# Kernel optimization log

Measured on AMD Instinct MI355X. Metric: run time of the kernel, lower is better.

Reference implementation:

```python
import jax, jax.numpy as jnp
import numpy as np

N_LAYER = 2
N_HEAD = 16
TOP_K = 2
CAPACITY = 1024  # B*T*top_k/num_experts * capacity_factor = 2*2048*2/8


def layer_norm(x, g, b, eps=1e-5):
    m = jnp.mean(x, axis=-1, keepdims=True)
    v = jnp.var(x, axis=-1, keepdims=True)
    return (x - m) * jax.lax.rsqrt(v + eps) * g + b


def attention(x, qkv_w, out_w):
    B, T, C = x.shape
    H, D = N_HEAD, C // N_HEAD
    qkv = (x @ qkv_w).reshape(B, T, 3, H, D)
    q, k, v = qkv[:, :, 0], qkv[:, :, 1], qkv[:, :, 2]
    scores = jnp.einsum('bthd,bshd->bhts', q, k) / jnp.sqrt(jnp.asarray(D, x.dtype))
    probs = jax.nn.softmax(scores, axis=-1)  # non-causal, dropout=0 (eval)
    o = jnp.einsum('bhts,bshd->bthd', probs, v).reshape(B, T, C)
    return o @ out_w


def sparse_moe(x, route_w, route_b, noise_w, noise_b, w1, b1, w2, b2, key):
    B, T, C = x.shape
    E = route_w.shape[-1]
    N = B * T
    flat = x.reshape(N, C)
    logits = flat @ route_w + route_b
    noise_logits = flat @ noise_w + noise_b
    noise = jax.random.normal(key, logits.shape, logits.dtype) * jax.nn.softplus(noise_logits)
    noisy = logits + noise
    topv, topi = jax.lax.top_k(noisy, TOP_K)            # [N,k]
    probs_k = jax.nn.softmax(topv, axis=-1)             # softmax over sparse(-inf) logits == softmax over top-k
    router = jnp.zeros_like(noisy).at[jnp.arange(N)[:, None], topi].set(probs_k)  # [N,E]
    # dispatch: per-expert token selection in token order, truncated at CAPACITY
    masks = (topi[None] == jnp.arange(E)[:, None, None]).any(-1)  # [E,N]
    order = jnp.argsort(~masks, axis=1, stable=True)[:, :CAPACITY]  # [E,cap] routed tokens first, in order
    valid = jnp.take_along_axis(masks, order, axis=1)               # [E,cap]
    gating = router[order, jnp.arange(E)[:, None]]                  # [E,cap]
    g = flat[order]                                                 # [E,cap,C]
    h = jax.nn.relu(jnp.einsum('ecd,edh->ech', g, w1) + b1[:, None])
    y = jnp.einsum('ech,ehd->ecd', h, w2) + b2[:, None]
    y = y * (gating * valid.astype(x.dtype))[..., None]
    upd = jnp.zeros_like(flat).at[order.reshape(-1)].add(y.reshape(-1, C))
    return upd.reshape(B, T, C)


def setup_inputs() -> dict:
    key = jax.random.key(0)
    ks = jax.random.split(key, 16)
    B, T, C, E, L, V = 2, 2048, 1024, 8, N_LAYER, 32000
    s = lambda fan: 1.0 / np.sqrt(fan)
    return {
        'input_ids': jax.random.randint(ks[0], (B, T), 0, V),
        'tok_emb': jax.random.normal(ks[1], (V, C), jnp.float32) * 0.02,
        'pos_emb': jax.random.normal(ks[2], (T, C), jnp.float32) * 0.02,
        'ln1_g': jnp.ones((L, C), jnp.float32), 'ln1_b': jnp.zeros((L, C), jnp.float32),
        'ln2_g': jnp.ones((L, C), jnp.float32), 'ln2_b': jnp.zeros((L, C), jnp.float32),
        'qkv_w': jax.random.normal(ks[3], (L, C, 3 * C), jnp.float32) * s(C),
        'out_w': jax.random.normal(ks[4], (L, C, C), jnp.float32) * s(C),
        'route_w': jax.random.normal(ks[5], (L, C, E), jnp.float32) * s(C),
        'route_b': jnp.zeros((L, E), jnp.float32),
        'noise_w': jax.random.normal(ks[6], (L, C, E), jnp.float32) * s(C),
        'noise_b': jnp.zeros((L, E), jnp.float32),
        'w1': jax.random.normal(ks[7], (L, E, C, 4 * C), jnp.float32) * s(C),
        'b1': jnp.zeros((L, E, 4 * C), jnp.float32),
        'w2': jax.random.normal(ks[8], (L, E, 4 * C, C), jnp.float32) * s(4 * C),
        'b2': jnp.zeros((L, E, C), jnp.float32),
        'lnf_g': jnp.ones((C,), jnp.float32), 'lnf_b': jnp.zeros((C,), jnp.float32),
        'head_w': jax.random.normal(ks[9], (C, 1), jnp.float32) * s(C),
        'head_b': jnp.zeros((1,), jnp.float32),
    }


def reference(input_ids, tok_emb, pos_emb, ln1_g, ln1_b, ln2_g, ln2_b, qkv_w, out_w,
              route_w, route_b, noise_w, noise_b, w1, b1, w2, b2, lnf_g, lnf_b, head_w, head_b):
    B, T = input_ids.shape
    x = tok_emb[input_ids] + pos_emb[:T]
    base = jax.random.key(42)
    for l in range(N_LAYER):
        x = x + attention(layer_norm(x, ln1_g[l], ln1_b[l]), qkv_w[l], out_w[l])
        moe = sparse_moe(layer_norm(x, ln2_g[l], ln2_b[l]), route_w[l], route_b[l],
                         noise_w[l], noise_b[l], w1[l], b1[l], w2[l], b2[l],
                         jax.random.fold_in(base, l))
        x = x + moe
    x = layer_norm(x, lnf_g, lnf_b)
    return x @ head_w + head_b  # [B,T,1]
```

## Files before the change

kernel.cpp:

```cpp
#include <hip/hip_runtime.h>
#include <stdint.h>
#include <math.h>

#define NTOK 4096
#define TSEQ 2048
#define CDIM 1024
#define NHEAD 16
#define DHEAD 64
#define NEXP 8
#define HIDN 4096
#define ECAP 1024

__device__ __forceinline__ void threefry2x32(uint32_t k0, uint32_t k1,
                                             uint32_t x0, uint32_t x1,
                                             uint32_t& o0, uint32_t& o1) {
  uint32_t ks2 = k0 ^ k1 ^ 0x1BD11BDAu;
#define TF_R(r) { x0 += x1; x1 = (x1 << (r)) | (x1 >> (32 - (r))); x1 ^= x0; }
  x0 += k0; x1 += k1;
  TF_R(13) TF_R(15) TF_R(26) TF_R(6)
  x0 += k1; x1 += ks2 + 1u;
  TF_R(17) TF_R(29) TF_R(16) TF_R(24)
  x0 += ks2; x1 += k0 + 2u;
  TF_R(13) TF_R(15) TF_R(26) TF_R(6)
  x0 += k0; x1 += k1 + 3u;
  TF_R(17) TF_R(29) TF_R(16) TF_R(24)
  x0 += k1; x1 += ks2 + 4u;
  TF_R(13) TF_R(15) TF_R(26) TF_R(6)
  x0 += ks2; x1 += k0 + 5u;
#undef TF_R
  o0 = x0; o1 = x1;
}

__device__ __forceinline__ float erfinv_f32(float x) {
  float w = -log1pf(-x * x);
  float p;
  if (w < 5.0f) {
    w = w - 2.5f;
    p = 2.81022636e-08f;
    p = fmaf(p, w, 3.43273939e-07f);
    p = fmaf(p, w, -3.5233877e-06f);
    p = fmaf(p, w, -4.39150654e-06f);
    p = fmaf(p, w, 0.00021858087f);
    p = fmaf(p, w, -0.00125372503f);
    p = fmaf(p, w, -0.00417768164f);
    p = fmaf(p, w, 0.246640727f);
    p = fmaf(p, w, 1.50140941f);
  } else {
    w = sqrtf(w) - 3.0f;
    p = -0.000200214257f;
    p = fmaf(p, w, 0.000100950558f);
    p = fmaf(p, w, 0.00134934322f);
    p = fmaf(p, w, -0.00367342844f);
    p = fmaf(p, w, 0.00573950773f);
    p = fmaf(p, w, -0.0076224613f);
    p = fmaf(p, w, 0.00943887047f);
    p = fmaf(p, w, 1.00167406f);
    p = fmaf(p, w, 2.83297682f);
  }
  return p * x;
}

__global__ __launch_bounds__(256) void k_embed(const int* __restrict__ ids,
    const float* __restrict__ tok, const float* __restrict__ pos,
    float* __restrict__ x) {
  int row = blockIdx.x;
  int id = ids[row];
  int t = row & (TSEQ - 1);
  const float* tr = tok + (size_t)id * CDIM;
  const float* pr = pos + (size_t)t * CDIM;
  float* xr = x + (size_t)row * CDIM;
  for (int c = threadIdx.x; c < CDIM; c += 256) xr[c] = tr[c] + pr[c];
}

__global__ __launch_bounds__(256) void k_ln(const float* __restrict__ in,
    float* __restrict__ out, const float* __restrict__ g, const float* __restrict__ b) {
  __shared__ float red[256];
  int row = blockIdx.x, tid = threadIdx.x;
  const float* xr = in + (size_t)row * CDIM;
  float s = 0.f;
  for (int c = tid; c < CDIM; c += 256) s += xr[c];
  red[tid] = s; __syncthreads();
  for (int off = 128; off > 0; off >>= 1) {
    if (tid < off) red[tid] += red[tid + off];
    __syncthreads();
  }
  float m = red[0] * (1.0f / CDIM);
  __syncthreads();
  float v = 0.f;
  for (int c = tid; c < CDIM; c += 256) { float d = xr[c] - m; v += d * d; }
  red[tid] = v; __syncthreads();
  for (int off = 128; off > 0; off >>= 1) {
    if (tid < off) red[tid] += red[tid + off];
    __syncthreads();
  }
  float var = red[0] * (1.0f / CDIM);
  float rstd = 1.0f / sqrtf(var + 1e-5f);
  float* orow = out + (size_t)row * CDIM;
  for (int c = tid; c < CDIM; c += 256)
    orow[c] = (xr[c] - m) * rstd * g[c] + b[c];
}

__global__ __launch_bounds__(256, 2) void k_gemm(
    const float* __restrict__ A, int lda,
    const float* __restrict__ B, int ldb,
    float* __restrict__ Cm, int ldc,
    int M, int N, int K,
    const float* __restrict__ bias,
    const int* __restrict__ gather,
    const int* __restrict__ countPtr,
    int flags,
    size_t zsA, size_t zsB, size_t zsC, int zsBias, int zsGather) {
  __shared__ float As[16][132];
  __shared__ float Bs[16][128];
  const int z = blockIdx.z;
  A += (size_t)z * zsA;
  B += (size_t)z * zsB;
  Cm += (size_t)z * zsC;
  if (bias) bias += (size_t)z * (size_t)zsBias;
  if (gather) gather += (size_t)z * (size_t)zsGather;
  int Meff = M;
  if (countPtr) { int cc = countPtr[z]; if (cc < Meff) Meff = cc; }
  const int row0 = blockIdx.y << 7, col0 = blockIdx.x << 7;
  if (row0 >= Meff) return;
  const int tid = threadIdx.x;
  const int tx = tid & 15, ty = tid >> 4;
  const int r0 = ty << 2, c0 = tx << 2;

  const int am0 = tid >> 2, ak0 = (tid & 3) << 2;
  const int am1 = am0 + 64, ak1 = ak0;
  const int bk0 = tid >> 5, bn0 = (tid & 31) << 2;
  const int bk1 = bk0 + 8,  bn1 = bn0;

  const int ag0 = row0 + am0, ag1 = row0 + am1;
  const float* aP0 = nullptr; const float* aP1 = nullptr;
  if (ag0 < Meff) aP0 = A + (size_t)(gather ? gather[ag0] : ag0) * lda + ak0;
  if (ag1 < Meff) aP1 = A + (size_t)(gather ? gather[ag1] : ag1) * lda + ak1;
  const float* bP0 = B + (size_t)bk0 * ldb + col0 + bn0;
  const float* bP1 = B + (size_t)bk1 * ldb + col0 + bn1;

  const float4 z4 = make_float4(0.f, 0.f, 0.f, 0.f);
  float4 aR0 = aP0 ? *(const float4*)aP0 : z4;
  float4 aR1 = aP1 ? *(const float4*)aP1 : z4;
  float4 bR0 = *(const float4*)bP0;
  float4 bR1 = *(const float4*)bP1;

  float acc[8][8];
#pragma unroll
  for (int i = 0; i < 8; ++i)
#pragma unroll
    for (int j = 0; j < 8; ++j) acc[i][j] = 0.f;

  for (int k0 = 0; k0 < K; k0 += 16) {
    As[ak0 + 0][am0] = aR0.x; As[ak0 + 1][am0] = aR0.y;
    As[ak0 + 2][am0] = aR0.z; As[ak0 + 3][am0] = aR0.w;
    As[ak1 + 0][am1] = aR1.x; As[ak1 + 1][am1] = aR1.y;
    As[ak1 + 2][am1] = aR1.z; As[ak1 + 3][am1] = aR1.w;
    *(float4*)&Bs[bk0][bn0] = bR0;
    *(float4*)&Bs[bk1][bn1] = bR1;
    __syncthreads();
    const int kn = k0 + 16;
    if (kn < K) {
      aR0 = aP0 ? *(const float4*)(aP0 + kn) : z4;
      aR1 = aP1 ? *(const float4*)(aP1 + kn) : z4;
      bR0 = *(const float4*)(bP0 + (size_t)kn * ldb);
      bR1 = *(const float4*)(bP1 + (size_t)kn * ldb);
    }
#pragma unroll
    for (int kk = 0; kk < 16; ++kk) {
      const float4 A0 = *(const float4*)&As[kk][r0];
      const float4 A1 = *(const float4*)&As[kk][r0 + 64];
      const float4 B0 = *(const float4*)&Bs[kk][c0];
      const float4 B1 = *(const float4*)&Bs[kk][c0 + 64];
      const float a[8] = {A0.x, A0.y, A0.z, A0.w, A1.x, A1.y, A1.z, A1.w};
      const float b[8] = {B0.x, B0.y, B0.z, B0.w, B1.x, B1.y, B1.z, B1.w};
#pragma unroll
      for (int i = 0; i < 8; ++i)
#pragma unroll
        for (int j = 0; j < 8; ++j) acc[i][j] = fmaf(a[i], b[j], acc[i][j]);
    }
    __syncthreads();
  }

#pragma unroll
  for (int ih = 0; ih < 2; ++ih) {
#pragma unroll
    for (int i = 0; i < 4; ++i) {
      int gr = row0 + r0 + ih * 64 + i;
      if (gr >= Meff) continue;
      float* crow = Cm + (size_t)gr * ldc + col0;
#pragma unroll
      for (int jh = 0; jh < 2; ++jh) {
        int cc = c0 + jh * 64;
        float4 v;
        v.x = acc[ih * 4 + i][jh * 4 + 0];
        v.y = acc[ih * 4 + i][jh * 4 + 1];
        v.z = acc[ih * 4 + i][jh * 4 + 2];
        v.w = acc[ih * 4 + i][jh * 4 + 3];
        if (bias) {
          v.x += bias[col0 + cc + 0]; v.y += bias[col0 + cc + 1];
          v.z += bias[col0 + cc + 2]; v.w += bias[col0 + cc + 3];
        }
        if (flags & 1) {
          v.x = fmaxf(v.x, 0.f); v.y = fmaxf(v.y, 0.f);
          v.z = fmaxf(v.z, 0.f); v.w = fmaxf(v.w, 0.f);
        }
        if (flags & 2) {
          float4 o = *(const float4*)&crow[cc];
          v.x += o.x; v.y += o.y; v.z += o.z; v.w += o.w;
        }
        *(float4*)&crow[cc] = v;
      }
    }
  }
}

__global__ __launch_bounds__(256, 1) void k_attn(const float* __restrict__ qkv,
                                                 float* __restrict__ o) {
  __shared__ float Qs[64][132];
  __shared__ float Ks[64][66];
  __shared__ float Vs[64][68];
  __shared__ float Ps[64][132];
  const int t0 = blockIdx.x << 7;
  const int h = blockIdx.y;
  const int b = blockIdx.z;
  const int tid = threadIdx.x;
  const int tx = tid & 15, ty = tid >> 4;
  const int r0 = ty << 2;
  const int c0 = tx << 2;

#pragma unroll
  for (int p = 0; p < 8; ++p) {
    int idx = tid + (p << 8);
    int r = idx >> 4, d4 = (idx & 15) << 2;
    const float4 q = *(const float4*)(qkv +
        ((size_t)(b * TSEQ + t0 + r) * 3 + 0) * CDIM + h * DHEAD + d4);
    Qs[d4 + 0][r] = q.x * 0.125f;
    Qs[d4 + 1][r] = q.y * 0.125f;
    Qs[d4 + 2][r] = q.z * 0.125f;
    Qs[d4 + 3][r] = q.w * 0.125f;
  }

  float m0[8], l0[8], Oacc[8][4];
#pragma unroll
  for (int i = 0; i < 8; ++i) {
    m0[i] = -INFINITY; l0[i] = 0.f;
#pragma unroll
    for (int j = 0; j < 4; ++j) Oacc[i][j] = 0.f;
  }

  float4 kreg[4], vreg[4];
#pragma unroll
  for (int p = 0; p < 4; ++p) {
    int idx = tid + (p << 8);
    int j = idx >> 4, d4 = (idx & 15) << 2;
    kreg[p] = *(const float4*)(qkv + ((size_t)(b * TSEQ + j) * 3 + 1) * CDIM + h * DHEAD + d4);
    vreg[p] = *(const float4*)(qkv + ((size_t)(b * TSEQ + j) * 3 + 2) * CDIM + h * DHEAD + d4);
  }

  for (int s0 = 0; s0 < TSEQ; s0 += 64) {
#pragma unroll
    for (int p = 0; p < 4; ++p) {
      int idx = tid + (p << 8);
      int j = idx >> 4, d4 = (idx & 15) << 2;
      Ks[d4 + 0][j] = kreg[p].x;
      Ks[d4 + 1][j] = kreg[p].y;
      Ks[d4 + 2][j] = kreg[p].z;
      Ks[d4 + 3][j] = kreg[p].w;
      *(float4*)&Vs[j][d4] = vreg[p];
    }
    __syncthreads();
    if (s0 + 64 < TSEQ) {
#pragma unroll
      for (int p = 0; p < 4; ++p) {
        int idx = tid + (p << 8);
        int j = idx >> 4, d4 = (idx & 15) << 2;
        kreg[p] = *(const float4*)(qkv + ((size_t)(b * TSEQ + s0 + 64 + j) * 3 + 1) * CDIM + h * DHEAD + d4);
        vreg[p] = *(const float4*)(qkv + ((size_t)(b * TSEQ + s0 + 64 + j) * 3 + 2) * CDIM + h * DHEAD + d4);
      }
    }
    float sacc[8][4];
#pragma unroll
    for (int i = 0; i < 8; ++i)
#pragma unroll
      for (int j = 0; j < 4; ++j) sacc[i][j] = 0.f;
#pragma unroll 8
    for (int kk = 0; kk < 64; ++kk) {
      const float4 qa = *(const float4*)&Qs[kk][r0];
      const float4 qb = *(const float4*)&Qs[kk][r0 + 64];
      const float2 ka = *(const float2*)&Ks[kk][c0];
      const float2 kb = *(const float2*)&Ks[kk][c0 + 2];
      const float av[8] = {qa.x, qa.y, qa.z, qa.w, qb.x, qb.y, qb.z, qb.w};
      const float bv[4] = {ka.x, ka.y, kb.x, kb.y};
#pragma unroll
      for (int i = 0; i < 8; ++i)
#pragma unroll
        for (int j = 0; j < 4; ++j) sacc[i][j] = fmaf(av[i], bv[j], sacc[i][j]);
    }
    float pv[8][4];
#pragma unroll
    for (int i = 0; i < 8; ++i) {
      float mx = fmaxf(fmaxf(sacc[i][0], sacc[i][1]), fmaxf(sacc[i][2], sacc[i][3]));
#pragma unroll
      for (int off = 8; off > 0; off >>= 1) mx = fmaxf(mx, __shfl_xor(mx, off, 16));
      float mnew = fmaxf(m0[i], mx);
      float alpha = expf(m0[i] - mnew);
      float psum = 0.f;
#pragma unroll
      for (int j = 0; j < 4; ++j) {
        float p = expf(sacc[i][j] - mnew);
        pv[i][j] = p;
        psum += p;
      }
#pragma unroll
      for (int off = 8; off > 0; off >>= 1) psum += __shfl_xor(psum, off, 16);
      l0[i] = l0[i] * alpha + psum;
      m0[i] = mnew;
#pragma unroll
      for (int j = 0; j < 4; ++j) Oacc[i][j] *= alpha;
    }
#pragma unroll
    for (int jj = 0; jj < 4; ++jj) {
      *(float4*)&Ps[c0 + jj][r0] =
          make_float4(pv[0][jj], pv[1][jj], pv[2][jj], pv[3][jj]);
      *(float4*)&Ps[c0 + jj][r0 + 64] =
          make_float4(pv[4][jj], pv[5][jj], pv[6][jj], pv[7][jj]);
    }
    __syncthreads();
#pragma unroll 8
    for (int kk = 0; kk < 64; ++kk) {
      const float4 pa = *(const float4*)&Ps[kk][r0];
      const float4 pb = *(const float4*)&Ps[kk][r0 + 64];
      const float4 vv = *(const float4*)&Vs[kk][c0];
      const float av[8] = {pa.x, pa.y, pa.z, pa.w, pb.x, pb.y, pb.z, pb.w};
      const float bv[4] = {vv.x, vv.y, vv.z, vv.w};
#pragma unroll
      for (int i = 0; i < 8; ++i)
#pragma unroll
        for (int j = 0; j < 4; ++j) Oacc[i][j] = fmaf(av[i], bv[j], Oacc[i][j]);
    }
    __syncthreads();
  }
#pragma unroll
  for (int i = 0; i < 8; ++i) {
    int r = t0 + ((i < 4) ? (r0 + i) : (r0 + 60 + i));
    float inv = 1.0f / l0[i];
    float4 v;
    v.x = Oacc[i][0] * inv; v.y = Oacc[i][1] * inv;
    v.z = Oacc[i][2] * inv; v.w = Oacc[i][3] * inv;
    *(float4*)(o + (size_t)(b * TSEQ + r) * CDIM + h * DHEAD + c0) = v;
  }
}

__global__ __launch_bounds__(256) void k_route(
    const float* __restrict__ xn,
    const float* __restrict__ rw, const float* __restrict__ rb,
    const float* __restrict__ nw, const float* __restrict__ nb,
    int layer, int* __restrict__ topi, float* __restrict__ gate) {
  int token = blockIdx.x, tid = threadIdx.x;
  float acc[16];
#pragma unroll
  for (int j = 0; j < 16; j++) acc[j] = 0.f;
  const float* xr = xn + (size_t)token * CDIM;
  for (int c = tid; c < CDIM; c += 256) {
    float xc = xr[c];
    const float* w1p = rw + (size_t)c * NEXP;
    const float* w2p = nw + (size_t)c * NEXP;
#pragma unroll
    for (int j = 0; j < 8; j++) acc[j] += xc * w1p[j];
#pragma unroll
    for (int j = 0; j < 8; j++) acc[8 + j] += xc * w2p[j];
  }
#pragma unroll
  for (int j = 0; j < 16; j++) {
#pragma unroll
    for (int off = 32; off > 0; off >>= 1) acc[j] += __shfl_xor(acc[j], off, 64);
  }
  __shared__ float wp[4][16];
  int wid = tid >> 6;
  if ((tid & 63) == 0) {
#pragma unroll
    for (int j = 0; j < 16; j++) wp[wid][j] = acc[j];
  }
  __syncthreads();
  __shared__ float noisy[8];
  if (tid < 8) {
    int j = tid;
    float logit = wp[0][j] + wp[1][j] + wp[2][j] + wp[3][j] + rb[j];
    float nl = wp[0][8 + j] + wp[1][8 + j] + wp[2][8 + j] + wp[3][8 + j] + nb[j];
    float sp = fmaxf(nl, 0.f) + log1pf(expf(-fabsf(nl)));
    uint32_t k0, k1, o0, o1;
    threefry2x32(0u, 42u, 0u, (uint32_t)layer, k0, k1);
    uint32_t idx = (uint32_t)(token * NEXP + j);
    threefry2x32(k0, k1, 0u, idx, o0, o1);
    uint32_t bits = o0 ^ o1;
    float f = __uint_as_float((bits >> 9) | 0x3f800000u) - 1.0f;
    const float lo = -0.99999994f;
    float u = fmaxf(lo, f * 2.0f + lo);
    float z = 1.41421356f * erfinv_f32(u);
    noisy[j] = logit + z * sp;
  }
  __syncthreads();
  if (tid == 0) {
    float v1 = -INFINITY; int i1 = 0;
#pragma unroll
    for (int j = 0; j < 8; j++) { float v = noisy[j]; if (v > v1) { v1 = v; i1 = j; } }
    float v2 = -INFINITY; int i2 = 0;
#pragma unroll
    for (int j = 0; j < 8; j++) {
      if (j == i1) continue;
      float v = noisy[j]; if (v > v2) { v2 = v; i2 = j; }
    }
    float e2 = expf(v2 - v1);
    float denom = 1.0f + e2;
    topi[token * 2] = i1; topi[token * 2 + 1] = i2;
    gate[token * 2] = 1.0f / denom;
    gate[token * 2 + 1] = e2 / denom;
  }
}

__global__ __launch_bounds__(256) void k_scan(const int* __restrict__ topi,
    int* __restrict__ perm, int* __restrict__ slot, int* __restrict__ count) {
  int e = blockIdx.x, tid = threadIdx.x;
  __shared__ int ps[256];
  __shared__ int sbase;
  if (tid == 0) sbase = 0;
  __syncthreads();
  for (int c0 = 0; c0 < NTOK; c0 += 256) {
    int token = c0 + tid;
    int j0 = topi[token * 2], j1 = topi[token * 2 + 1];
    int flag = (j0 == e || j1 == e) ? 1 : 0;
    ps[tid] = flag;
    __syncthreads();
    for (int off = 1; off < 256; off <<= 1) {
      int v = (tid >= off) ? ps[tid - off] : 0;
      __syncthreads();
      ps[tid] += v;
      __syncthreads();
    }
    int pos = sbase + ps[tid] - flag;
    if (flag) {
      int s = (pos < ECAP) ? pos : -1;
      if (s >= 0) perm[e * ECAP + s] = token;
      if (j0 == e) slot[token * 2] = s;
      else slot[token * 2 + 1] = s;
    }
    __syncthreads();
    if (tid == 0) sbase += ps[255];
    __syncthreads();
  }
  if (tid == 0) count[e] = (sbase < ECAP) ? sbase : ECAP;
}

__global__ __launch_bounds__(256) void k_moe_add(
    const float* __restrict__ ybuf,
    const int* __restrict__ topi, const int* __restrict__ slot,
    const float* __restrict__ gate, float* __restrict__ x) {
  int token = blockIdx.x, tid = threadIdx.x;
  int e0 = topi[token * 2], s0 = slot[token * 2];
  int e1 = topi[token * 2 + 1], s1 = slot[token * 2 + 1];
  float g0 = gate[token * 2], g1 = gate[token * 2 + 1];
  const float* y0 = ybuf + ((size_t)e0 * ECAP + (s0 < 0 ? 0 : s0)) * CDIM;
  const float* y1 = ybuf + ((size_t)e1 * ECAP + (s1 < 0 ? 0 : s1)) * CDIM;
  float* xr = x + (size_t)token * CDIM;
  for (int c = tid; c < CDIM; c += 256) {
    float v = xr[c];
    if (s0 >= 0) v += g0 * y0[c];
    if (s1 >= 0) v += g1 * y1[c];
    xr[c] = v;
  }
}

__global__ __launch_bounds__(256) void k_head(const float* __restrict__ xn,
    const float* __restrict__ hw, const float* __restrict__ hb,
    float* __restrict__ out) {
  __shared__ float red[256];
  int token = blockIdx.x, tid = threadIdx.x;
  const float* xr = xn + (size_t)token * CDIM;
  float s = 0.f;
  for (int c = tid; c < CDIM; c += 256) s += xr[c] * hw[c];
  red[tid] = s; __syncthreads();
  for (int off = 128; off > 0; off >>= 1) {
    if (tid < off) red[tid] += red[tid + off];
    __syncthreads();
  }
  if (tid == 0) out[token] = red[0] + hb[0];
}

extern "C" void kernel_launch(void* const* d_in, const int* in_sizes, int n_in,
                              void* d_out, int out_size, void* d_ws, size_t ws_size,
                              hipStream_t stream) {
  const int* ids = (const int*)d_in[0];
  const float* tok_emb = (const float*)d_in[1];
  const float* pos_emb = (const float*)d_in[2];
  const float* ln1_g = (const float*)d_in[3];
  const float* ln1_b = (const float*)d_in[4];
  const float* ln2_g = (const float*)d_in[5];
  const float* ln2_b = (const float*)d_in[6];
  const float* qkv_w = (const float*)d_in[7];
  const float* out_w = (const float*)d_in[8];
  const float* route_w = (const float*)d_in[9];
  const float* route_b = (const float*)d_in[10];
  const float* noise_w = (const float*)d_in[11];
  const float* noise_b = (const float*)d_in[12];
  const float* w1 = (const float*)d_in[13];
  const float* b1 = (const float*)d_in[14];
  const float* w2 = (const float*)d_in[15];
  const float* b2 = (const float*)d_in[16];
  const float* lnf_g = (const float*)d_in[17];
  const float* lnf_b = (const float*)d_in[18];
  const float* head_w = (const float*)d_in[19];
  const float* head_b = (const float*)d_in[20];
  float* out = (float*)d_out;

  const size_t MB = 1024u * 1024u;
  char* ws = (char*)d_ws;
  const bool big = ws_size >= (size_t)194 * MB;

  float* x    = (float*)(ws);
  float* xn   = (float*)(ws + 16 * MB);
  float* qkv  = (float*)(ws + 32 * MB);
  float* hbuf = (float*)(ws + 32 * MB);
  float* ybuf = big ? (float*)(ws + 160 * MB)
                    : (float*)(ws + 48 * MB);
  char* small = big ? (ws + 192 * MB) : (ws + 80 * MB);
  int* topi = (int*)small;
  int* slot = topi + 2 * NTOK;
  float* gate = (float*)(slot + 2 * NTOK);
  int* perm = (int*)(gate + 2 * NTOK);
  int* count = perm + NEXP * ECAP;

  k_embed<<<NTOK, 256, 0, stream>>>(ids, tok_emb, pos_emb, x);

  for (int l = 0; l < 2; l++) {
    k_ln<<<NTOK, 256, 0, stream>>>(x, xn, ln1_g + l * CDIM, ln1_b + l * CDIM);
    k_gemm<<<dim3(3 * CDIM / 128, NTOK / 128, 1), 256, 0, stream>>>(xn, CDIM,
        qkv_w + (size_t)l * CDIM * 3 * CDIM, 3 * CDIM, qkv, 3 * CDIM,
        NTOK, 3 * CDIM, CDIM, nullptr, nullptr, nullptr, 0,
        0, 0, 0, 0, 0);
    k_attn<<<dim3(TSEQ / 128, NHEAD, 2), 256, 0, stream>>>(qkv, xn);
    k_gemm<<<dim3(CDIM / 128, NTOK / 128, 1), 256, 0, stream>>>(xn, CDIM,
        out_w + (size_t)l * CDIM * CDIM, CDIM, x, CDIM,
        NTOK, CDIM, CDIM, nullptr, nullptr, nullptr, 2,
        0, 0, 0, 0, 0);
    k_ln<<<NTOK, 256, 0, stream>>>(x, xn, ln2_g + l * CDIM, ln2_b + l * CDIM);
    k_route<<<NTOK, 256, 0, stream>>>(xn,
        route_w + (size_t)l * CDIM * NEXP, route_b + l * NEXP,
        noise_w + (size_t)l * CDIM * NEXP, noise_b + l * NEXP,
        l, topi, gate);
    k_scan<<<NEXP, 256, 0, stream>>>(topi, perm, slot, count);
    if (big) {
      k_gemm<<<dim3(HIDN / 128, ECAP / 128, NEXP), 256, 0, stream>>>(xn, CDIM,
          w1 + (size_t)l * NEXP * CDIM * HIDN, HIDN, hbuf, HIDN,
          ECAP, HIDN, CDIM, b1 + (size_t)l * NEXP * HIDN, perm, count, 1,
          0, (size_t)CDIM * HIDN, (size_t)ECAP * HIDN, HIDN, ECAP);
      k_gemm<<<dim3(CDIM / 128, ECAP / 128, NEXP), 256, 0, stream>>>(hbuf, HIDN,
          w2 + (size_t)l * NEXP * HIDN * CDIM, CDIM, ybuf, CDIM,
          ECAP, CDIM, HIDN, b2 + (size_t)l * NEXP * CDIM, nullptr, count, 0,
          (size_t)ECAP * HIDN, (size_t)HIDN * CDIM, (size_t)ECAP * CDIM, CDIM, 0);
    } else {
      for (int e = 0; e < NEXP; e++) {
        const size_t we = (size_t)(l * NEXP + e);
        k_gemm<<<dim3(HIDN / 128, ECAP / 128, 1), 256, 0, stream>>>(xn, CDIM,
            w1 + we * CDIM * HIDN, HIDN, hbuf, HIDN,
            ECAP, HIDN, CDIM, b1 + we * HIDN, perm + e * ECAP, count + e, 1,
            0, 0, 0, 0, 0);
        k_gemm<<<dim3(CDIM / 128, ECAP / 128, 1), 256, 0, stream>>>(hbuf, HIDN,
            w2 + we * HIDN * CDIM, CDIM, ybuf + (size_t)e * ECAP * CDIM, CDIM,
            ECAP, CDIM, HIDN, b2 + we * CDIM, nullptr, count + e, 0,
            0, 0, 0, 0, 0);
      }
    }
    k_moe_add<<<NTOK, 256, 0, stream>>>(ybuf, topi, slot, gate, x);
  }

  k_ln<<<NTOK, 256, 0, stream>>>(x, xn, lnf_g, lnf_b);
  k_head<<<NTOK, 256, 0, stream>>>(xn, head_w, head_b, out);
}
```

Before: 5.856 ms.

## Use split-bf16 MFMA (3-pass) in GEMM kernel instead of FP32 FMA

Replaces the FP32 SIMT outer-product GEMM with matrix-core MFMA 16x16x32 bf16 instructions. Each FP32 operand is split into a bf16 high and low part, and three products (hh, hl, lh) are accumulated to approximate FP32 precision. Shared-memory tiles are reorganised into k-contiguous bf16 layouts with a K step of 32. The aim is to move the dominant GEMM cost onto the matrix cores. In exchange, accuracy drops slightly relative to exact FP32, and the epilogue now writes scalars instead of float4 stores.

```diff
diff --git a/kernel.cpp b/kernel.cpp
--- a/kernel.cpp
+++ b/kernel.cpp
@@ -10,6 +10,9 @@
 #define NEXP 8
 #define HIDN 4096
 #define ECAP 1024
+
+typedef short bf16x8 __attribute__((ext_vector_type(8)));
+typedef float f32x4 __attribute__((ext_vector_type(4)));
 
 __device__ __forceinline__ void threefry2x32(uint32_t k0, uint32_t k1,
                                              uint32_t x0, uint32_t x1,
@@ -60,6 +63,16 @@
   return p * x;
 }
 
+__device__ __forceinline__ void split2(float x0, float x1,
+                                       uint32_t& hi, uint32_t& lo) {
+  uint32_t h, l;
+  asm("v_cvt_pk_bf16_f32 %0, %1, %2" : "=v"(h) : "v"(x0), "v"(x1));
+  float h0 = __uint_as_float(h << 16);
+  float h1 = __uint_as_float(h & 0xffff0000u);
+  asm("v_cvt_pk_bf16_f32 %0, %1, %2" : "=v"(l) : "v"(x0 - h0), "v"(x1 - h1));
+  hi = h; lo = l;
+}
+
 __global__ __launch_bounds__(256) void k_embed(const int* __restrict__ ids,
     const float* __restrict__ tok, const float* __restrict__ pos,
     float* __restrict__ x) {
@@ -110,8 +123,10 @@
     const int* __restrict__ countPtr,
     int flags,
     size_t zsA, size_t zsB, size_t zsC, int zsBias, int zsGather) {
-  __shared__ float As[16][132];
-  __shared__ float Bs[16][128];
+  __shared__ short Ah[128][40];
+  __shared__ short Al[128][40];
+  __shared__ short Bh[128][40];
+  __shared__ short Bl[128][40];
   const int z = blockIdx.z;
   A += (size_t)z * zsA;
   B += (size_t)z * zsB;
@@ -123,92 +138,111 @@
   const int row0 = blockIdx.y << 7, col0 = blockIdx.x << 7;
   if (row0 >= Meff) return;
   const int tid = threadIdx.x;
-  const int tx = tid & 15, ty = tid >> 4;
-  const int r0 = ty << 2, c0 = tx << 2;
-
-  const int am0 = tid >> 2, ak0 = (tid & 3) << 2;
-  const int am1 = am0 + 64, ak1 = ak0;
-  const int bk0 = tid >> 5, bn0 = (tid & 31) << 2;
-  const int bk1 = bk0 + 8,  bn1 = bn0;
-
-  const int ag0 = row0 + am0, ag1 = row0 + am1;
-  const float* aP0 = nullptr; const float* aP1 = nullptr;
-  if (ag0 < Meff) aP0 = A + (size_t)(gather ? gather[ag0] : ag0) * lda + ak0;
-  if (ag1 < Meff) aP1 = A + (size_t)(gather ? gather[ag1] : ag1) * lda + ak1;
-  const float* bP0 = B + (size_t)bk0 * ldb + col0 + bn0;
-  const float* bP1 = B + (size_t)bk1 * ldb + col0 + bn1;
+
+  const int ar = tid >> 1, ak = (tid & 1) << 4;
+  const int bk = (tid >> 5) << 2, bc = (tid & 31) << 2;
+
+  const int agrow = row0 + ar;
+  const float* aP = nullptr;
+  if (agrow < Meff) aP = A + (size_t)(gather ? gather[agrow] : agrow) * lda + ak;
+  const float* bP = B + (size_t)bk * ldb + col0 + bc;
 
   const float4 z4 = make_float4(0.f, 0.f, 0.f, 0.f);
-  float4 aR0 = aP0 ? *(const float4*)aP0 : z4;
-  float4 aR1 = aP1 ? *(const float4*)aP1 : z4;
-  float4 bR0 = *(const float4*)bP0;
-  float4 bR1 = *(const float4*)bP1;
-
-  float acc[8][8];
-#pragma unroll
-  for (int i = 0; i < 8; ++i)
-#pragma unroll
-    for (int j = 0; j < 8; ++j) acc[i][j] = 0.f;
-
-  for (int k0 = 0; k0 < K; k0 += 16) {
-    As[ak0 + 0][am0] = aR0.x; As[ak0 + 1][am0] = aR0.y;
-    As[ak0 + 2][am0] = aR0.z; As[ak0 + 3][am0] = aR0.w;
-    As[ak1 + 0][am1] = aR1.x; As[ak1 + 1][am1] = aR1.y;
-    As[ak1 + 2][am1] = aR1.z; As[ak1 + 3][am1] = aR1.w;
-    *(float4*)&Bs[bk0][bn0] = bR0;
-    *(float4*)&Bs[bk1][bn1] = bR1;
-    __syncthreads();
-    const int kn = k0 + 16;
+  float4 aR[4], bR[4];
+#pragma unroll
+  for (int j = 0; j < 4; ++j) {
+    aR[j] = aP ? *(const float4*)(aP + (j << 2)) : z4;
+    bR[j] = *(const float4*)(bP + (size_t)j * ldb);
+  }
+
+  const int lane = tid & 63, wv = tid >> 6;
+  const int wr = (wv >> 1) << 6, wc = (wv & 1) << 6;
+  const int lr = lane & 15;
+  const int k8 = (lane >> 4) << 3;
+  const int qrow = (lane >> 4) << 2;
+
+  f32x4 acc[4][4];
+#pragma unroll
+  for (int i = 0; i < 4; ++i)
+#pragma unroll
+    for (int j = 0; j < 4; ++j) acc[i][j] = (f32x4)0.f;
+
+  for (int k0 = 0; k0 < K; k0 += 32) {
+    {
+      uint32_t h[8], l[8];
+      split2(aR[0].x, aR[0].y, h[0], l[0]);
+      split2(aR[0].z, aR[0].w, h[1], l[1]);
+      split2(aR[1].x, aR[1].y, h[2], l[2]);
+      split2(aR[1].z, aR[1].w, h[3], l[3]);
+      split2(aR[2].x, aR[2].y, h[4], l[4]);
+      split2(aR[2].z, aR[2].w, h[5], l[5]);
+      split2(aR[3].x, aR[3].y, h[6], l[6]);
+      split2(aR[3].z, aR[3].w, h[7], l[7]);
+      *(uint4*)&Ah[ar][ak]     = make_uint4(h[0], h[1], h[2], h[3]);
+      *(uint4*)&Ah[ar][ak + 8] = make_uint4(h[4], h[5], h[6], h[7]);
+      *(uint4*)&Al[ar][ak]     = make_uint4(l[0], l[1], l[2], l[3]);
+      *(uint4*)&Al[ar][ak + 8] = make_uint4(l[4], l[5], l[6], l[7]);
+    }
+    {
+      uint32_t h01, l01, h23, l23;
+      split2(bR[0].x, bR[1].x, h01, l01); split2(bR[2].x, bR[3].x, h23, l23);
+      *(uint2*)&Bh[bc + 0][bk] = make_uint2(h01, h23);
+      *(uint2*)&Bl[bc + 0][bk] = make_uint2(l01, l23);
+      split2(bR[0].y, bR[1].y, h01, l01); split2(bR[2].y, bR[3].y, h23, l23);
+      *(uint2*)&Bh[bc + 1][bk] = make_uint2(h01, h23);
+      *(uint2*)&Bl[bc + 1][bk] = make_uint2(l01, l23);
+      split2(bR[0].z, bR[1].z, h01, l01); split2(bR[2].z, bR[3].z, h23, l23);
+      *(uint2*)&Bh[bc + 2][bk] = make_uint2(h01, h23);
+      *(uint2*)&Bl[bc + 2][bk] = make_uint2(l01, l23);
+      split2(bR[0].w, bR[1].w, h01, l01); split2(bR[2].w, bR[3].w, h23, l23);
+      *(uint2*)&Bh[bc + 3][bk] = make_uint2(h01, h23);
+      *(uint2*)&Bl[bc + 3][bk] = make_uint2(l01, l23);
+    }
+    __syncthreads();
+    const int kn = k0 + 32;
     if (kn < K) {
-      aR0 = aP0 ? *(const float4*)(aP0 + kn) : z4;
-      aR1 = aP1 ? *(const float4*)(aP1 + kn) : z4;
-      bR0 = *(const float4*)(bP0 + (size_t)kn * ldb);
-      bR1 = *(const float4*)(bP1 + (size_t)kn * ldb);
-    }
-#pragma unroll
-    for (int kk = 0; kk < 16; ++kk) {
-      const float4 A0 = *(const float4*)&As[kk][r0];
-      const float4 A1 = *(const float4*)&As[kk][r0 + 64];
-      const float4 B0 = *(const float4*)&Bs[kk][c0];
-      const float4 B1 = *(const float4*)&Bs[kk][c0 + 64];
-      const float a[8] = {A0.x, A0.y, A0.z, A0.w, A1.x, A1.y, A1.z, A1.w};
-      const float b[8] = {B0.x, B0.y, B0.z, B0.w, B1.x, B1.y, B1.z, B1.w};
-#pragma unroll
-      for (int i = 0; i < 8; ++i)
-#pragma unroll
-        for (int j = 0; j < 8; ++j) acc[i][j] = fmaf(a[i], b[j], acc[i][j]);
-    }
-    __syncthreads();
-  }
-
-#pragma unroll
-  for (int ih = 0; ih < 2; ++ih) {
-#pragma unroll
-    for (int i = 0; i < 4; ++i) {
-      int gr = row0 + r0 + ih * 64 + i;
-      if (gr >= Meff) continue;
-      float* crow = Cm + (size_t)gr * ldc + col0;
-#pragma unroll
-      for (int jh = 0; jh < 2; ++jh) {
-        int cc = c0 + jh * 64;
-        float4 v;
-        v.x = acc[ih * 4 + i][jh * 4 + 0];
-        v.y = acc[ih * 4 + i][jh * 4 + 1];
-        v.z = acc[ih * 4 + i][jh * 4 + 2];
-        v.w = acc[ih * 4 + i][jh * 4 + 3];
-        if (bias) {
-          v.x += bias[col0 + cc + 0]; v.y += bias[col0 + cc + 1];
-          v.z += bias[col0 + cc + 2]; v.w += bias[col0 + cc + 3];
-        }
-        if (flags & 1) {
-          v.x = fmaxf(v.x, 0.f); v.y = fmaxf(v.y, 0.f);
-          v.z = fmaxf(v.z, 0.f); v.w = fmaxf(v.w, 0.f);
-        }
-        if (flags & 2) {
-          float4 o = *(const float4*)&crow[cc];
-          v.x += o.x; v.y += o.y; v.z += o.z; v.w += o.w;
-        }
-        *(float4*)&crow[cc] = v;
+#pragma unroll
+      for (int j = 0; j < 4; ++j) {
+        aR[j] = aP ? *(const float4*)(aP + kn + (j << 2)) : z4;
+        bR[j] = *(const float4*)(bP + (size_t)(kn + j) * ldb);
+      }
+    }
+    bf16x8 vbh[4], vbl[4];
+#pragma unroll
+    for (int nt = 0; nt < 4; ++nt) {
+      vbh[nt] = *(const bf16x8*)&Bh[wc + nt * 16 + lr][k8];
+      vbl[nt] = *(const bf16x8*)&Bl[wc + nt * 16 + lr][k8];
+    }
+#pragma unroll
+    for (int mt = 0; mt < 4; ++mt) {
+      const bf16x8 vah = *(const bf16x8*)&Ah[wr + mt * 16 + lr][k8];
+      const bf16x8 val = *(const bf16x8*)&Al[wr + mt * 16 + lr][k8];
+#pragma unroll
+      for (int nt = 0; nt < 4; ++nt) {
+        acc[mt][nt] = __builtin_amdgcn_mfma_f32_16x16x32_bf16(vah, vbh[nt], acc[mt][nt], 0, 0, 0);
+        acc[mt][nt] = __builtin_amdgcn_mfma_f32_16x16x32_bf16(vah, vbl[nt], acc[mt][nt], 0, 0, 0);
+        acc[mt][nt] = __builtin_amdgcn_mfma_f32_16x16x32_bf16(val, vbh[nt], acc[mt][nt], 0, 0, 0);
+      }
+    }
+    __syncthreads();
+  }
+
+#pragma unroll
+  for (int mt = 0; mt < 4; ++mt) {
+#pragma unroll
+    for (int nt = 0; nt < 4; ++nt) {
+      const int gc = col0 + wc + nt * 16 + lr;
+      const int gr0 = row0 + wr + mt * 16 + qrow;
+#pragma unroll
+      for (int q = 0; q < 4; ++q) {
+        const int gr = gr0 + q;
+        if (gr >= Meff) continue;
+        float v = acc[mt][nt][q];
+        if (bias) v += bias[gc];
+        if (flags & 1) v = fmaxf(v, 0.f);
+        float* cp = Cm + (size_t)gr * ldc + gc;
+        if (flags & 2) v += *cp;
+        *cp = v;
       }
     }
   }
```

Measured after the change: 4.853 ms. -17.1%, faster.
